# Kernel optimization log

Measured on AMD Instinct MI355X. Metric: run time of the kernel, lower is better.

The kernel has to match this reference:

```python
import jax, jax.numpy as jnp
import numpy as np

N, D, E, K = 65536, 2048, 64, 8
EPS = 1e-5


def setup_inputs() -> dict:
    key = jax.random.key(0)
    kx, kw = jax.random.split(key)
    x = jax.random.normal(kx, (N, D), dtype=jnp.float32)
    # nn.Linear(input_size, num_experts, bias=False) weight: [E, D]
    W = jax.random.normal(kw, (E, D), dtype=jnp.float32) * (1.0 / np.sqrt(D))
    return {"x": x, "W": W}


def _l1_normalize(v):
    # torch F.normalize(p=1, dim=0): v / max(||v||_1, 1e-12)
    return v / jnp.maximum(jnp.sum(jnp.abs(v)), 1e-12)


def reference(x, W):
    # router logits: [N, E] in float32 (matches .float() in torch code)
    logits = (x @ W.T).astype(jnp.float32)
    top_v, top_i = jax.lax.top_k(logits, K)            # [N, K]
    top_k_gates = jax.nn.softmax(top_v, axis=-1).astype(x.dtype)
    # training-branch aux loss (compute_aux_loss)
    probs = jax.nn.softmax(logits, axis=-1)            # [N, E]
    rows = jnp.arange(logits.shape[0])[:, None]
    dense_gates = jnp.zeros_like(probs, dtype=top_k_gates.dtype).at[rows, top_i].set(top_k_gates)
    probs_sum = probs.sum(0)                           # [E]
    freq = (dense_gates > 0).astype(jnp.float32).sum(0)  # [E]
    # log(sum(exp(logits)) + eps)^2 summed, computed stably
    lse = jnp.logaddexp(jax.scipy.special.logsumexp(logits, axis=-1), jnp.log(EPS))
    zloss = jnp.sum(lse ** 2) / logits.shape[0]
    switchloss = E * jnp.sum(_l1_normalize(probs_sum) * _l1_normalize(freq))
    loss = switchloss + 0.1 * zloss
    return top_i, top_k_gates, loss
```

## Files before the change

### kernel.cpp

```cpp
#include <hip/hip_runtime.h>
#include <math.h>

#define NROWS 65536
#define DDIM 2048
#define NEXP 64
#define TOPK 8

constexpr int NSTEP = 64;
constexpr float THR = 3e-4f;
constexpr int WFRAG_STEP = 4096;

typedef short bf16x8 __attribute__((ext_vector_type(8)));
typedef float f32x4 __attribute__((ext_vector_type(4)));

__device__ inline unsigned short bfround(float f) {
    union { float f; unsigned u; } v; v.f = f;
    unsigned r = (v.u + 0x7fffu + ((v.u >> 16) & 1u)) >> 16;
    return (unsigned short)r;
}
__device__ inline float bf2f(unsigned short h) {
    union { unsigned u; float f; } v; v.u = ((unsigned)h) << 16;
    return v.f;
}
__device__ inline void cvt8(const float4& A, const float4& B, bf16x8& h, bf16x8& l) {
    float f[8] = {A.x, A.y, A.z, A.w, B.x, B.y, B.z, B.w};
#pragma unroll
    for (int j = 0; j < 8; ++j) {
        unsigned short hh = bfround(f[j]);
        h[j] = (short)hh;
        l[j] = (short)bfround(f[j] - bf2f(hh));
    }
}

__global__ __launch_bounds__(256)
void prep_kernel(const float* __restrict__ W, short* __restrict__ wfrag)
{
    const int t = blockIdx.x;
    const int tid = threadIdx.x;
    const int ct = tid >> 6, lane = tid & 63;
    const int e = ct * 16 + (lane & 15);
    const int k = t * 32 + (lane >> 4) * 8;
    const float* wp = W + (size_t)e * DDIM + k;
    float4 a = *reinterpret_cast<const float4*>(wp);
    float4 b = *reinterpret_cast<const float4*>(wp + 4);
    bf16x8 h, l;
    cvt8(a, b, h, l);
    short* base = wfrag + (size_t)t * WFRAG_STEP;
    *reinterpret_cast<bf16x8*>(base + (ct * 64 + lane) * 8) = h;
    *reinterpret_cast<bf16x8*>(base + 2048 + (ct * 64 + lane) * 8) = l;
}

__global__ __launch_bounds__(256, 2)
void gemm_kernel(const float* __restrict__ x, const short* __restrict__ wfrag,
                 float* __restrict__ logits)
{
    __shared__ __align__(16) short Bfrag[2][2][4][64][8];

    const int tid = threadIdx.x;
    const int w = tid >> 6;
    const int lane = tid & 63;
    const int g = lane >> 4;
    const int c = lane & 15;
    const int row0 = blockIdx.x * 64 + w * 16;
    const float* xr = x + (size_t)(row0 + c) * DDIM + g * 8;

    const int se = tid >> 2, skg = tid & 3;
    const int sct = se >> 4;
    const int slane = (se & 15) + (skg << 4);
    const int soff = (sct * 64 + slane) * 8;

    auto stageB = [&](int t, int buf) {
        const short* src = wfrag + (size_t)t * WFRAG_STEP + soff;
        *reinterpret_cast<bf16x8*>(&Bfrag[buf][0][sct][slane][0]) =
            *reinterpret_cast<const bf16x8*>(src);
        *reinterpret_cast<bf16x8*>(&Bfrag[buf][1][sct][slane][0]) =
            *reinterpret_cast<const bf16x8*>(src + 2048);
    };

    f32x4 acc[4];
#pragma unroll
    for (int ct = 0; ct < 4; ++ct) acc[ct] = (f32x4){0.f, 0.f, 0.f, 0.f};

    float4 xa0 = *reinterpret_cast<const float4*>(xr);
    float4 xa1 = *reinterpret_cast<const float4*>(xr + 4);
    float4 xb0, xb1;
    stageB(0, 0);
    __syncthreads();

    for (int t = 0; t < NSTEP; ++t) {
        const int buf = t & 1;
        const int kn = (t + 1) * 32;
        if (t + 1 < NSTEP) {
            xb0 = *reinterpret_cast<const float4*>(xr + kn);
            xb1 = *reinterpret_cast<const float4*>(xr + kn + 4);
            stageB(t + 1, buf ^ 1);
        }
        bf16x8 ah, al;
        cvt8(xa0, xa1, ah, al);
#pragma unroll
        for (int ct = 0; ct < 4; ++ct) {
            bf16x8 bh = *reinterpret_cast<const bf16x8*>(&Bfrag[buf][0][ct][lane][0]);
            bf16x8 bl = *reinterpret_cast<const bf16x8*>(&Bfrag[buf][1][ct][lane][0]);
            acc[ct] = __builtin_amdgcn_mfma_f32_16x16x32_bf16(ah, bh, acc[ct], 0, 0, 0);
            acc[ct] = __builtin_amdgcn_mfma_f32_16x16x32_bf16(ah, bl, acc[ct], 0, 0, 0);
            acc[ct] = __builtin_amdgcn_mfma_f32_16x16x32_bf16(al, bh, acc[ct], 0, 0, 0);
        }
        xa0 = xb0; xa1 = xb1;
        __syncthreads();
    }

#pragma unroll
    for (int ct = 0; ct < 4; ++ct)
#pragma unroll
        for (int reg = 0; reg < 4; ++reg)
            logits[(size_t)(row0 + g * 4 + reg) * NEXP + ct * 16 + c] = acc[ct][reg];
}

__global__ __launch_bounds__(256, 2)
void epilogue_kernel(const float* __restrict__ x, const float* __restrict__ W,
                     const float* __restrict__ logits,
                     float* __restrict__ out_idx, float* __restrict__ out_gate,
                     float* __restrict__ g_psum, float* __restrict__ g_freq,
                     float* __restrict__ g_zsum)
{
    __shared__ float psum_s[NEXP];
    __shared__ float fcnt_s[NEXP];
    __shared__ float zsq_s;
    const int tid = threadIdx.x;
    const int w = tid >> 6;
    const int lane = tid & 63;
    if (tid < NEXP) { psum_s[tid] = 0.f; fcnt_s[tid] = 0.f; }
    if (tid == 0) zsq_s = 0.f;
    __syncthreads();

    const int wi = blockIdx.x * 4 + w;
    float pcol = 0.f, zacc = 0.f;

    for (int r8 = 0; r8 < 8; ++r8) {
        const int row = wi + r8 * 8192;
        const float lg = logits[(size_t)row * NEXP + lane];

        unsigned u = __float_as_uint(lg);
        unsigned ordb = (u & 0x80000000u) ? ~u : (u | 0x80000000u);
        unsigned long long key =
            ((unsigned long long)ordb << 32) | (unsigned)(63 - lane);

#pragma unroll
        for (int k = 2; k <= 64; k <<= 1) {
#pragma unroll
            for (int j = k >> 1; j > 0; j >>= 1) {
                unsigned long long other = __shfl_xor(key, j, 64);
                const bool keep_max = ((lane & j) == 0) == ((lane & k) == 0);
                const bool mine_bigger = key > other;
                key = (keep_max == mine_bigger) ? key : other;
            }
        }
        unsigned ou = (unsigned)(key >> 32);
        unsigned ub = (ou & 0x80000000u) ? (ou ^ 0x80000000u) : ~ou;
        const float val = __uint_as_float(ub);
        const int idxe = 63 - (int)(key & 63u);

        const float m0 = __shfl(val, 0, 64);

        float pe = expf(lg - m0);
        float s = pe;
#pragma unroll
        for (int m = 1; m < 64; m <<= 1) s += __shfl_xor(s, m, 64);
        pcol += pe / s;

        if (lane == 0) {
            float lsef = m0 + logf(s);
            const float lb = -11.512925464970229f;
            float mx = fmaxf(lsef, lb), mn = fminf(lsef, lb);
            float z = mx + log1pf(expf(mn - mx));
            zacc += z * z;
        }

        float nxt = __shfl_down(val, 1, 64);
        float dg = (lane < 8) ? (val - nxt) : 3.4e38f;
        float mg = dg;
#pragma unroll
        for (int m = 1; m < 8; m <<= 1) mg = fminf(mg, __shfl_xor(mg, m, 8));
        mg = __shfl(mg, 0, 64);
        const float v9 = __shfl(val, 8, 64);
        const size_t base = (size_t)row * TOPK;

        if (mg >= THR) {
            float eg = expf(val - m0);
            float gs = eg;
#pragma unroll
            for (int m = 1; m < 8; m <<= 1) gs += __shfl_xor(gs, m, 8);
            if (lane < 8) {
                out_idx[base + lane] = (float)idxe;
                out_gate[base + lane] = eg / gs;
                atomicAdd(&fcnt_s[idxe], 1.f);
            }
        } else {
            const bool cand = (lg >= v9 - THR);
            unsigned long long cm = __ballot(cand);
            const float* xrw = x + (size_t)row * DDIM;
            float4 xv[8];
#pragma unroll
            for (int j = 0; j < 8; ++j)
                xv[j] = *reinterpret_cast<const float4*>(xrw + j * 256 + lane * 4);

            double myD = -HUGE_VAL;
            unsigned long long m2 = cm;
            while (m2) {
                const int e = (int)__ffsll((unsigned long long)m2) - 1;
                m2 &= (m2 - 1);
                const float* wrp = W + (size_t)e * DDIM;
                double p0 = 0.0, p1 = 0.0, p2 = 0.0, p3 = 0.0;
#pragma unroll
                for (int j = 0; j < 8; ++j) {
                    float4 wv = *reinterpret_cast<const float4*>(wrp + j * 256 + lane * 4);
                    p0 = fma((double)xv[j].x, (double)wv.x, p0);
                    p1 = fma((double)xv[j].y, (double)wv.y, p1);
                    p2 = fma((double)xv[j].z, (double)wv.z, p2);
                    p3 = fma((double)xv[j].w, (double)wv.w, p3);
                }
                double sd = (p0 + p1) + (p2 + p3);
#pragma unroll
                for (int m = 1; m < 64; m <<= 1) sd += __shfl_xor(sd, m, 64);
                if (lane == e) myD = sd;
            }

            double v = cand ? myD : -HUGE_VAL;
            double tvd[8]; int ti8[8];
#pragma unroll
            for (int p = 0; p < 8; ++p) {
                double bv = v; int bgi = lane;
#pragma unroll
                for (int m = 1; m < 64; m <<= 1) {
                    double ov = __shfl_xor(bv, m, 64);
                    int ogi = __shfl_xor(bgi, m, 64);
                    if (ov > bv || (ov == bv && ogi < bgi)) { bv = ov; bgi = ogi; }
                }
                tvd[p] = bv; ti8[p] = bgi;
                if (lane == bgi) v = -HUGE_VAL;
            }
            const double m0d = tvd[0];
            double gsum = 0.0, ge[8];
#pragma unroll
            for (int j = 0; j < 8; ++j) { ge[j] = exp(tvd[j] - m0d); gsum += ge[j]; }
            if (lane < 8) {
                double myge = ge[0]; int myti = ti8[0];
#pragma unroll
                for (int j = 1; j < 8; ++j)
                    if (lane == j) { myge = ge[j]; myti = ti8[j]; }
                out_idx[base + lane] = (float)myti;
                out_gate[base + lane] = (float)(myge / gsum);
                atomicAdd(&fcnt_s[myti], 1.f);
            }
        }
    }

    atomicAdd(&psum_s[lane], pcol);
    if (lane == 0) atomicAdd(&zsq_s, zacc);
    __syncthreads();
    if (tid < NEXP) {
        atomicAdd(&g_psum[tid], psum_s[tid]);
        atomicAdd(&g_freq[tid], fcnt_s[tid]);
    }
    if (tid == 0) atomicAdd(g_zsum, zsq_s);
}

__global__ void finalize_kernel(const float* __restrict__ g_psum,
                                const float* __restrict__ g_freq,
                                const float* __restrict__ g_zsum,
                                float* __restrict__ out_loss)
{
    const int lane = threadIdx.x & 63;
    float p = g_psum[lane], f = g_freq[lane];
    float sp = p, sf = f;
#pragma unroll
    for (int m = 1; m < 64; m <<= 1) { sp += __shfl_xor(sp, m, 64); sf += __shfl_xor(sf, m, 64); }
    sp = fmaxf(sp, 1e-12f);
    sf = fmaxf(sf, 1e-12f);
    float term = (p / sp) * (f / sf);
#pragma unroll
    for (int m = 1; m < 64; m <<= 1) term += __shfl_xor(term, m, 64);
    if (lane == 0)
        out_loss[0] = (float)NEXP * term + 0.1f * (g_zsum[0] / (float)NROWS);
}

extern "C" void kernel_launch(void* const* d_in, const int* in_sizes, int n_in,
                              void* d_out, int out_size, void* d_ws, size_t ws_size,
                              hipStream_t stream)
{
    const float* x = (const float*)d_in[0];
    const float* W = (const float*)d_in[1];
    float* out = (float*)d_out;
    float* out_idx  = out;
    float* out_gate = out + (size_t)NROWS * TOPK;
    float* out_loss = out + (size_t)2 * NROWS * TOPK;

    float* acc    = (float*)d_ws;
    float* logits = (float*)d_ws + 256;
    short* wfrag  = (short*)((float*)d_ws + 256 + (size_t)NROWS * NEXP);
    hipMemsetAsync(d_ws, 0, 129 * sizeof(float), stream);

    prep_kernel<<<NSTEP, 256, 0, stream>>>(W, wfrag);
    gemm_kernel<<<NROWS / 64, 256, 0, stream>>>(x, wfrag, logits);
    epilogue_kernel<<<2048, 256, 0, stream>>>(x, W, logits, out_idx, out_gate,
                                              acc, acc + NEXP, acc + 2 * NEXP);
    finalize_kernel<<<1, 64, 0, stream>>>(acc, acc + NEXP, acc + 2 * NEXP, out_loss);
}
```

Baseline: 282.3 us.

## Process four rows per wavefront with 16-lane top-k and deferred fp64 fallback

The epilogue now maps four rows onto one wavefront, 16 lanes per row with 4 logits each and a float4 load, and finds the top-9 by repeated 16-lane argmax instead of a full 64-lane bitonic sort. Rows whose top-8 gaps fall below the threshold are placed in a per-wave shared list and recomputed afterwards in fp64 using the old full-wave path. This is meant to cut shuffle and sort cost per row and make logits reads contiguous, since each wave now handles 8 consecutive rows. The trade-offs are more register use, and the flagged rows now run as a serial second pass in which each wave waits on its own rows only.

```diff
diff --git a/kernel.cpp b/kernel.cpp
--- a/kernel.cpp
+++ b/kernel.cpp
@@ -126,25 +126,101 @@
     __shared__ float psum_s[NEXP];
     __shared__ float fcnt_s[NEXP];
     __shared__ float zsq_s;
+    __shared__ int fList[4][8];
+    __shared__ int fN[4];
     const int tid = threadIdx.x;
     const int w = tid >> 6;
     const int lane = tid & 63;
+    const int g = lane >> 4;
+    const int c = lane & 15;
     if (tid < NEXP) { psum_s[tid] = 0.f; fcnt_s[tid] = 0.f; }
     if (tid == 0) zsq_s = 0.f;
+    if (lane == 0) fN[w] = 0;
     __syncthreads();
 
     const int wi = blockIdx.x * 4 + w;
-    float pcol = 0.f, zacc = 0.f;
-
-    for (int r8 = 0; r8 < 8; ++r8) {
-        const int row = wi + r8 * 8192;
+    float pcol[4] = {0.f, 0.f, 0.f, 0.f};
+    float zacc = 0.f;
+
+    for (int it = 0; it < 2; ++it) {
+        const int row = wi * 8 + it * 4 + g;
+        float4 Lv = *reinterpret_cast<const float4*>(&logits[(size_t)row * NEXP + c * 4]);
+        float L[4] = {Lv.x, Lv.y, Lv.z, Lv.w};
+        float ld[4] = {L[0], L[1], L[2], L[3]};
+
+        float tv[9]; int ti[9];
+#pragma unroll
+        for (int p = 0; p < 9; ++p) {
+            float bv = -3.4e38f; int bgi = 127;
+#pragma unroll
+            for (int j = 0; j < 4; ++j) {
+                int e = c * 4 + j;
+                if (ld[j] > bv) { bv = ld[j]; bgi = e; }
+            }
+#pragma unroll
+            for (int m = 1; m < 16; m <<= 1) {
+                float ov = __shfl_xor(bv, m, 16);
+                int ogi = __shfl_xor(bgi, m, 16);
+                if (ov > bv || (ov == bv && ogi < bgi)) { bv = ov; bgi = ogi; }
+            }
+            tv[p] = bv; ti[p] = bgi;
+#pragma unroll
+            for (int j = 0; j < 4; ++j)
+                if (bgi == c * 4 + j) ld[j] = -3.4e38f;
+        }
+
+        const float m0 = tv[0];
+        float pe[4], ps = 0.f;
+#pragma unroll
+        for (int j = 0; j < 4; ++j) { pe[j] = expf(L[j] - m0); ps += pe[j]; }
+        float s = ps;
+#pragma unroll
+        for (int m = 1; m < 16; m <<= 1) s += __shfl_xor(s, m, 16);
+        const float inv_s = 1.f / s;
+#pragma unroll
+        for (int j = 0; j < 4; ++j) pcol[j] += pe[j] * inv_s;
+
+        if (c == 0) {
+            float lsef = m0 + logf(s);
+            const float lb = -11.512925464970229f;
+            float mx = fmaxf(lsef, lb), mn = fminf(lsef, lb);
+            float z = mx + log1pf(expf(mn - mx));
+            zacc += z * z;
+        }
+
+        float mg = 3.4e38f;
+#pragma unroll
+        for (int p = 0; p < 8; ++p) mg = fminf(mg, tv[p] - tv[p + 1]);
+        const bool flagged = (mg < THR);
+        const size_t base = (size_t)row * TOPK;
+
+        float gs = 0.f;
+#pragma unroll
+        for (int p = 0; p < 8; ++p) gs += expf(tv[p] - m0);
+        if (c < 8) {
+            float mytv = tv[0]; int myti = ti[0];
+#pragma unroll
+            for (int p = 1; p < 8; ++p)
+                if (c == p) { mytv = tv[p]; myti = ti[p]; }
+            out_idx[base + c] = (float)myti;
+            out_gate[base + c] = expf(mytv - m0) / gs;
+            if (!flagged) atomicAdd(&fcnt_s[myti], 1.f);
+        }
+        if (flagged && c == 0) {
+            int sl = atomicAdd(&fN[w], 1);
+            fList[w][sl] = row;
+        }
+    }
+
+    const int nf = fN[w];
+    for (int si = 0; si < nf; ++si) {
+        const int row = fList[w][si];
         const float lg = logits[(size_t)row * NEXP + lane];
 
         unsigned u = __float_as_uint(lg);
         unsigned ordb = (u & 0x80000000u) ? ~u : (u | 0x80000000u);
         unsigned long long key =
             ((unsigned long long)ordb << 32) | (unsigned)(63 - lane);
-
 #pragma unroll
         for (int k = 2; k <= 64; k <<= 1) {
 #pragma unroll
@@ -158,105 +234,70 @@
         unsigned ou = (unsigned)(key >> 32);
         unsigned ub = (ou & 0x80000000u) ? (ou ^ 0x80000000u) : ~ou;
         const float val = __uint_as_float(ub);
-        const int idxe = 63 - (int)(key & 63u);
-
-        const float m0 = __shfl(val, 0, 64);
-
-        float pe = expf(lg - m0);
-        float s = pe;
-#pragma unroll
-        for (int m = 1; m < 64; m <<= 1) s += __shfl_xor(s, m, 64);
-        pcol += pe / s;
-
-        if (lane == 0) {
-            float lsef = m0 + logf(s);
-            const float lb = -11.512925464970229f;
-            float mx = fmaxf(lsef, lb), mn = fminf(lsef, lb);
-            float z = mx + log1pf(expf(mn - mx));
-            zacc += z * z;
-        }
-
-        float nxt = __shfl_down(val, 1, 64);
-        float dg = (lane < 8) ? (val - nxt) : 3.4e38f;
-        float mg = dg;
-#pragma unroll
-        for (int m = 1; m < 8; m <<= 1) mg = fminf(mg, __shfl_xor(mg, m, 8));
-        mg = __shfl(mg, 0, 64);
         const float v9 = __shfl(val, 8, 64);
-        const size_t base = (size_t)row * TOPK;
-
-        if (mg >= THR) {
-            float eg = expf(val - m0);
-            float gs = eg;
-#pragma unroll
-            for (int m = 1; m < 8; m <<= 1) gs += __shfl_xor(gs, m, 8);
-            if (lane < 8) {
-                out_idx[base + lane] = (float)idxe;
-                out_gate[base + lane] = eg / gs;
-                atomicAdd(&fcnt_s[idxe], 1.f);
-            }
-        } else {
-            const bool cand = (lg >= v9 - THR);
-            unsigned long long cm = __ballot(cand);
-            const float* xrw = x + (size_t)row * DDIM;
-            float4 xv[8];
-#pragma unroll
-            for (int j = 0; j < 8; ++j)
-                xv[j] = *reinterpret_cast<const float4*>(xrw + j * 256 + lane * 4);
-
-            double myD = -HUGE_VAL;
-            unsigned long long m2 = cm;
-            while (m2) {
-                const int e = (int)__ffsll((unsigned long long)m2) - 1;
-                m2 &= (m2 - 1);
-                const float* wrp = W + (size_t)e * DDIM;
-                double p0 = 0.0, p1 = 0.0, p2 = 0.0, p3 = 0.0;
-#pragma unroll
-                for (int j = 0; j < 8; ++j) {
-                    float4 wv = *reinterpret_cast<const float4*>(wrp + j * 256 + lane * 4);
-                    p0 = fma((double)xv[j].x, (double)wv.x, p0);
-                    p1 = fma((double)xv[j].y, (double)wv.y, p1);
-                    p2 = fma((double)xv[j].z, (double)wv.z, p2);
-                    p3 = fma((double)xv[j].w, (double)wv.w, p3);
-                }
-                double sd = (p0 + p1) + (p2 + p3);
-#pragma unroll
-                for (int m = 1; m < 64; m <<= 1) sd += __shfl_xor(sd, m, 64);
-                if (lane == e) myD = sd;
-            }
-
-            double v = cand ? myD : -HUGE_VAL;
-            double tvd[8]; int ti8[8];
-#pragma unroll
-            for (int p = 0; p < 8; ++p) {
-                double bv = v; int bgi = lane;
-#pragma unroll
-                for (int m = 1; m < 64; m <<= 1) {
-                    double ov = __shfl_xor(bv, m, 64);
-                    int ogi = __shfl_xor(bgi, m, 64);
-                    if (ov > bv || (ov == bv && ogi < bgi)) { bv = ov; bgi = ogi; }
-                }
-                tvd[p] = bv; ti8[p] = bgi;
-                if (lane == bgi) v = -HUGE_VAL;
-            }
-            const double m0d = tvd[0];
-            double gsum = 0.0, ge[8];
-#pragma unroll
-            for (int j = 0; j < 8; ++j) { ge[j] = exp(tvd[j] - m0d); gsum += ge[j]; }
-            if (lane < 8) {
-                double myge = ge[0]; int myti = ti8[0];
-#pragma unroll
-                for (int j = 1; j < 8; ++j)
-                    if (lane == j) { myge = ge[j]; myti = ti8[j]; }
-                out_idx[base + lane] = (float)myti;
-                out_gate[base + lane] = (float)(myge / gsum);
-                atomicAdd(&fcnt_s[myti], 1.f);
-            }
-        }
-    }
-
-    atomicAdd(&psum_s[lane], pcol);
-    if (lane == 0) atomicAdd(&zsq_s, zacc);
+
+        const bool cand = (lg >= v9 - THR);
+        unsigned long long cm = __ballot(cand);
+        const float* xrw = x + (size_t)row * DDIM;
+        float4 xv[8];
+#pragma unroll
+        for (int j = 0; j < 8; ++j)
+            xv[j] = *reinterpret_cast<const float4*>(xrw + j * 256 + lane * 4);
+
+        double myD = -HUGE_VAL;
+        unsigned long long m2 = cm;
+        while (m2) {
+            const int e = (int)__ffsll((unsigned long long)m2) - 1;
+            m2 &= (m2 - 1);
+            const float* wrp = W + (size_t)e * DDIM;
+            double p0 = 0.0, p1 = 0.0, p2 = 0.0, p3 = 0.0;
+#pragma unroll
+            for (int j = 0; j < 8; ++j) {
+                float4 wv = *reinterpret_cast<const float4*>(wrp + j * 256 + lane * 4);
+                p0 = fma((double)xv[j].x, (double)wv.x, p0);
+                p1 = fma((double)xv[j].y, (double)wv.y, p1);
+                p2 = fma((double)xv[j].z, (double)wv.z, p2);
+                p3 = fma((double)xv[j].w, (double)wv.w, p3);
+            }
+            double sd = (p0 + p1) + (p2 + p3);
+#pragma unroll
+            for (int m = 1; m < 64; m <<= 1) sd += __shfl_xor(sd, m, 64);
+            if (lane == e) myD = sd;
+        }
+
+        double v = cand ? myD : -HUGE_VAL;
+        double tvd[8]; int ti8[8];
+#pragma unroll
+        for (int p = 0; p < 8; ++p) {
+            double bv = v; int bgi = lane;
+#pragma unroll
+            for (int m = 1; m < 64; m <<= 1) {
+                double ov = __shfl_xor(bv, m, 64);
+                int ogi = __shfl_xor(bgi, m, 64);
+                if (ov > bv || (ov == bv && ogi < bgi)) { bv = ov; bgi = ogi; }
+            }
+            tvd[p] = bv; ti8[p] = bgi;
+            if (lane == bgi) v = -HUGE_VAL;
+        }
+        const double m0d = tvd[0];
+        double gsum = 0.0, ge[8];
+#pragma unroll
+        for (int j = 0; j < 8; ++j) { ge[j] = exp(tvd[j] - m0d); gsum += ge[j]; }
+        if (lane < 8) {
+            double myge = ge[0]; int myti = ti8[0];
+#pragma unroll
+            for (int j = 1; j < 8; ++j)
+                if (lane == j) { myge = ge[j]; myti = ti8[j]; }
+            const size_t base = (size_t)row * TOPK;
+            out_idx[base + lane] = (float)myti;
+            out_gate[base + lane] = (float)(myge / gsum);
+            atomicAdd(&fcnt_s[myti], 1.f);
+        }
+    }
+
+#pragma unroll
+    for (int j = 0; j < 4; ++j) atomicAdd(&psum_s[c * 4 + j], pcol[j]);
+    if (c == 0) atomicAdd(&zsq_s, zacc);
     __syncthreads();
     if (tid < NEXP) {
         atomicAdd(&g_psum[tid], psum_s[tid]);
```

New measurement: 264.7 us. -6.2%, faster.
